# Optimization experiments

Measured on AMD Instinct MI355X. Metric: run time of the kernel, lower is better.

The kernel has to match this reference:

```python
import jax, jax.numpy as jnp
import numpy as np

B = 8192      # batch
LAT = 256     # latent_dimension
HID = 512     # hidden_size
INP = 128     # input_size (n_layer_types + 1 feature)
T = 64        # max_length
MLP = 512     # fixed MLP width in source


def _lin(key, fan_in, fan_out):
    kw, kb = jax.random.split(key)
    s = 1.0 / np.sqrt(fan_in)
    W = jax.random.uniform(kw, (fan_in, fan_out), jnp.float32, -s, s)
    b = jax.random.uniform(kb, (fan_out,), jnp.float32, -s, s)
    return W, b


def setup_inputs() -> dict:
    key = jax.random.key(0)
    ks = jax.random.split(key, 16)
    x = jax.random.normal(ks[0], (B, LAT), jnp.float32)
    W1, b1 = _lin(ks[1], LAT, MLP)
    W2, b2 = _lin(ks[2], MLP, MLP)
    W3, b3 = _lin(ks[3], MLP, MLP)
    Wh1, bh1 = _lin(ks[4], MLP, MLP)
    Wh2, bh2 = _lin(ks[5], MLP, HID)
    Wc1, bc1 = _lin(ks[6], MLP, MLP)
    Wc2, bc2 = _lin(ks[7], MLP, HID)
    Wx1, bx1 = _lin(ks[8], MLP, MLP)
    Wx2, bx2 = _lin(ks[9], MLP, INP)
    Wih, bih = _lin(ks[10], INP, 4 * HID)   # LSTM input->gates (i,f,g,o)
    Whh, bhh = _lin(ks[11], HID, 4 * HID)   # LSTM hidden->gates
    Wp, bp = _lin(ks[12], HID, INP)          # predictor head
    return dict(x=x, W1=W1, b1=b1, W2=W2, b2=b2, W3=W3, b3=b3,
                Wh1=Wh1, bh1=bh1, Wh2=Wh2, bh2=bh2,
                Wc1=Wc1, bc1=bc1, Wc2=Wc2, bc2=bc2,
                Wx1=Wx1, bx1=bx1, Wx2=Wx2, bx2=bx2,
                Wih=Wih, bih=bih, Whh=Whh, bhh=bhh, Wp=Wp, bp=bp)


def _lrelu(v):
    return jnp.where(v >= 0, v, 0.2 * v)


def _head(v):
    # split [d-1, 1]: softmax over layer types, sigmoid on feature scalar
    lt = jax.nn.softmax(v[..., :-1], axis=-1)
    ft = jax.nn.sigmoid(v[..., -1:])
    return jnp.concatenate([lt, ft], axis=-1)


def reference(x, W1, b1, W2, b2, W3, b3, Wh1, bh1, Wh2, bh2,
              Wc1, bc1, Wc2, bc2, Wx1, bx1, Wx2, bx2,
              Wih, bih, Whh, bhh, Wp, bp):
    z = _lrelu(x @ W1 + b1)
    z = _lrelu(z @ W2 + b2)
    z = _lrelu(z @ W3 + b3)
    h = _lrelu(z @ Wh1 + bh1) @ Wh2 + bh2          # [B, HID]
    c = _lrelu(z @ Wc1 + bc1) @ Wc2 + bc2          # [B, HID]
    x0 = _head(_lrelu(z @ Wx1 + bx1) @ Wx2 + bx2)  # [B, INP]

    def step(carry, _):
        xt, h, c = carry
        g = xt @ Wih + h @ Whh + (bih + bhh)        # [B, 4*HID]
        i, f, gg, o = jnp.split(g, 4, axis=-1)      # torch gate order i,f,g,o
        c2 = jax.nn.sigmoid(f) * c + jax.nn.sigmoid(i) * jnp.tanh(gg)
        h2 = jax.nn.sigmoid(o) * jnp.tanh(c2)
        nxt = _head(h2 @ Wp + bp)
        return (nxt, h2, c2), nxt

    # The torch loop reruns the LSTM over the growing prefix with the same
    # initial (h,c) and takes the last output; by LSTM causality this equals
    _, ys = jax.lax.scan(step, (x0, h, c), None, length=T)
    return jnp.transpose(ys, (1, 0, 2))  # [B, T, INP]
```

## Files before the change

kernel.cpp:

```cpp
#include <hip/hip_runtime.h>


typedef _Float16 h16;
typedef __attribute__((ext_vector_type(8))) _Float16 f16x8;
typedef __attribute__((ext_vector_type(4))) float f32x4;

#define BB 8192
#define TT 64

__device__ __forceinline__ void gload16(const void* g, void* lds) {
  __builtin_amdgcn_global_load_lds(
      (const __attribute__((address_space(1))) unsigned int*)g,
      (__attribute__((address_space(3))) unsigned int*)lds, 16, 0, 0);
}

__device__ __forceinline__ float sigm(float x) { return 1.f / (1.f + __expf(-x)); }
__device__ __forceinline__ float tanhf_(float x) { return 2.f / (1.f + __expf(-2.f * x)) - 1.f; }

#define MIDBAR_LG()                                        \
  do {                                                     \
    __builtin_amdgcn_s_barrier();                          \
    asm volatile("s_waitcnt lgkmcnt(0)" ::: "memory");     \
    __builtin_amdgcn_sched_barrier(0);                     \
  } while (0)
#define ENDBAR()                                           \
  do {                                                     \
    __builtin_amdgcn_s_barrier();                          \
    asm volatile("" ::: "memory");                         \
  } while (0)

__global__ __launch_bounds__(512, 2) void gate8(
    const h16* __restrict__ A, const h16* __restrict__ Bt,
    const float* __restrict__ bg, float* __restrict__ Cbuf,
    h16* __restrict__ Hout) {
  __shared__ __align__(16) h16 As[2][256 * 64];
  __shared__ __align__(16) h16 Bs[2][256 * 64];
  const int tid = threadIdx.x;
  const int lane = tid & 63;
  const int wid = tid >> 6;
  const int wr = wid >> 2, wc = wid & 3;
  const int m0 = blockIdx.x * 256;
  const int n0 = blockIdx.y * 256;
  const int arow = lane & 15, khi = lane >> 4;
  const int x7 = arow & 7;

  auto stage = [&](h16(*dst)[256 * 64], int slot, int h, const h16* src,
                   int base, int kt) {
#pragma unroll
    for (int li = 0; li < 2; ++li) {
      int rowbase = li * 128 + h * 64 + wid * 8;
      int row = rowbase + (lane >> 3);
      int gc = (lane & 7) ^ (lane >> 3);
      gload16(src + (size_t)(base + row) * 640 + kt * 64 + gc * 8,
              &dst[slot][rowbase * 64]);
    }
  };

  f32x4 acc[8][4];
#pragma unroll
  for (int i = 0; i < 8; ++i)
#pragma unroll
    for (int j = 0; j < 4; ++j) acc[i][j] = (f32x4)0.f;
  f16x8 af[4], bf[2][4];

  auto readA = [&](int slot, int ms, int ks) {
#pragma unroll
    for (int mr = 0; mr < 4; ++mr) {
      int r = wr * 128 + ms * 64 + mr * 16 + arow;
      af[mr] = *(const f16x8*)&As[slot][r * 64 + ((ks * 4 + khi) ^ x7) * 8];
    }
  };
  auto readB = [&](int slot, int ks) {
#pragma unroll
    for (int j = 0; j < 4; ++j) {
      int rb = wc * 64 + j * 16 + arow;
      bf[ks][j] = *(const f16x8*)&Bs[slot][rb * 64 + ((ks * 4 + khi) ^ x7) * 8];
    }
  };
  auto mfma16 = [&](int ms, int ks) {
    __builtin_amdgcn_s_setprio(1);
#pragma unroll
    for (int mr = 0; mr < 4; ++mr)
#pragma unroll
      for (int j = 0; j < 4; ++j)
        acc[ms * 4 + mr][j] = __builtin_amdgcn_mfma_f32_16x16x32_f16(
            af[mr], bf[ks][j], acc[ms * 4 + mr][j], 0, 0, 0);
    __builtin_amdgcn_s_setprio(0);
  };

  stage(Bs, 0, 0, Bt, n0, 0);
  stage(Bs, 0, 1, Bt, n0, 0);
  stage(As, 0, 0, A, m0, 0);
  stage(As, 0, 1, A, m0, 0);
  stage(Bs, 1, 0, Bt, n0, 1);
  stage(Bs, 1, 1, Bt, n0, 1);
  stage(As, 1, 0, A, m0, 1);
  asm volatile("s_waitcnt vmcnt(6)" ::: "memory");
  ENDBAR();

#pragma unroll 1
  for (int i = 0; i < 5; ++i) {
    const int t2 = 2 * i + 2, t3 = 2 * i + 3;
    readB(0, 0);
    readB(0, 1);
    readA(0, 0, 0);
    stage(As, 1, 1, A, m0, 2 * i + 1);
    MIDBAR_LG();
    mfma16(0, 0);
    ENDBAR();
    readA(0, 0, 1);
    if (t2 < 10) stage(Bs, 0, 0, Bt, n0, t2);
    MIDBAR_LG();
    mfma16(0, 1);
    ENDBAR();
    readA(0, 1, 0);
    if (t2 < 10) stage(Bs, 0, 1, Bt, n0, t2);
    MIDBAR_LG();
    mfma16(1, 0);
    ENDBAR();
    readA(0, 1, 1);
    if (t2 < 10) stage(As, 0, 0, A, m0, t2);
    if (i < 4)
      asm volatile("s_waitcnt vmcnt(6)" ::: "memory");
    else
      asm volatile("s_waitcnt vmcnt(0)" ::: "memory");
    MIDBAR_LG();
    mfma16(1, 1);
    ENDBAR();
    readB(1, 0);
    readB(1, 1);
    readA(1, 0, 0);
    if (t2 < 10) stage(As, 0, 1, A, m0, t2);
    MIDBAR_LG();
    mfma16(0, 0);
    ENDBAR();
    readA(1, 0, 1);
    if (t3 < 10) stage(Bs, 1, 0, Bt, n0, t3);
    MIDBAR_LG();
    mfma16(0, 1);
    ENDBAR();
    readA(1, 1, 0);
    if (t3 < 10) stage(Bs, 1, 1, Bt, n0, t3);
    MIDBAR_LG();
    mfma16(1, 0);
    ENDBAR();
    readA(1, 1, 1);
    if (t3 < 10) stage(As, 1, 0, A, m0, t3);
    if (i < 4)
      asm volatile("s_waitcnt vmcnt(6)" ::: "memory");
    else
      asm volatile("s_waitcnt vmcnt(0)" ::: "memory");
    MIDBAR_LG();
    mfma16(1, 1);
    ENDBAR();
  }

  const int hj = blockIdx.y * 64 + wc * 16 + arow;
  const int nb = n0 + wc * 64;
  const float bI = bg[nb + arow];
  const float bF = bg[nb + 16 + arow];
  const float bG = bg[nb + 32 + arow];
  const float bO = bg[nb + 48 + arow];
#pragma unroll
  for (int mrep = 0; mrep < 8; ++mrep) {
#pragma unroll
    for (int r = 0; r < 4; ++r) {
      int m = m0 + wr * 128 + mrep * 16 + khi * 4 + r;
      float gi = sigm(acc[mrep][0][r] + bI);
      float gf = sigm(acc[mrep][1][r] + bF);
      float gg = tanhf_(acc[mrep][2][r] + bG);
      float go = sigm(acc[mrep][3][r] + bO);
      size_t ci = (size_t)m * 512 + hj;
      float c2 = gf * Cbuf[ci] + gi * gg;
      Cbuf[ci] = c2;
      Hout[(size_t)m * 640 + 128 + hj] = (h16)(go * tanhf_(c2));
    }
  }
}

__global__ __launch_bounds__(256) void head_gemm2(
    const h16* __restrict__ A, int lda, const h16* __restrict__ Bt,
    const float* __restrict__ bias, int nkt, h16* __restrict__ Xout,
    float* __restrict__ ydst, int tstep) {
  __shared__ __align__(16) h16 As[2][64 * 64];
  __shared__ __align__(16) h16 Bs[2][128 * 64];
  const int tid = threadIdx.x;
  const int lane = tid & 63;
  const int w = tid >> 6;
  const int m0 = blockIdx.x * 64;
  const int arow = lane & 15, khi = lane >> 4;
  const int x7 = arow & 7;

  auto stageA = [&](int slot, int kt) {
#pragma unroll
    for (int li = 0; li < 2; ++li) {
      int rowbase = li * 32 + w * 8;
      int row = rowbase + (lane >> 3);
      int gc = (lane & 7) ^ (lane >> 3);
      gload16(A + (size_t)(m0 + row) * lda + kt * 64 + gc * 8,
              &As[slot][rowbase * 64]);
    }
  };
  auto stageB = [&](int slot, int kt) {
#pragma unroll
    for (int li = 0; li < 4; ++li) {
      int rowbase = li * 32 + w * 8;
      int row = rowbase + (lane >> 3);
      int gc = (lane & 7) ^ (lane >> 3);
      gload16(Bt + (size_t)row * 512 + kt * 64 + gc * 8,
              &Bs[slot][rowbase * 64]);
    }
  };

  f32x4 acc[8];
#pragma unroll
  for (int j = 0; j < 8; ++j) acc[j] = (f32x4)0.f;

  stageA(0, 0);
  stageB(0, 0);
#pragma unroll 1
  for (int kt = 0; kt < nkt; ++kt) {
    int p = kt & 1;
    if (kt + 1 < nkt) {
      stageA(p ^ 1, kt + 1);
      stageB(p ^ 1, kt + 1);
      asm volatile("s_waitcnt vmcnt(6)" ::: "memory");
    } else {
      asm volatile("s_waitcnt vmcnt(0)" ::: "memory");
    }
    ENDBAR();
#pragma unroll
    for (int kk = 0; kk < 2; ++kk) {
      int kc = kk * 4 + khi;
      int ra = w * 16 + arow;
      f16x8 afr = *(const f16x8*)&As[p][ra * 64 + (kc ^ x7) * 8];
#pragma unroll
      for (int nt = 0; nt < 8; ++nt) {
        int rb = nt * 16 + arow;
        f16x8 bfr = *(const f16x8*)&Bs[p][rb * 64 + (kc ^ x7) * 8];
        acc[nt] = __builtin_amdgcn_mfma_f32_16x16x32_f16(afr, bfr, acc[nt], 0, 0, 0);
      }
    }
    ENDBAR();
  }

#pragma unroll
  for (int r = 0; r < 4; ++r) {
    int m = m0 + w * 16 + khi * 4 + r;
    float v[8];
    float mx = -1e30f;
#pragma unroll
    for (int nt = 0; nt < 8; ++nt) {
      int col = nt * 16 + arow;
      v[nt] = acc[nt][r] + bias[col];
      if (col != 127) mx = fmaxf(mx, v[nt]);
    }
#pragma unroll
    for (int s = 1; s < 16; s <<= 1) mx = fmaxf(mx, __shfl_xor(mx, s, 16));
    float sm = 0.f;
#pragma unroll
    for (int nt = 0; nt < 8; ++nt) {
      int col = nt * 16 + arow;
      if (col != 127) sm += __expf(v[nt] - mx);
    }
#pragma unroll
    for (int s = 1; s < 16; s <<= 1) sm += __shfl_xor(sm, s, 16);
    float inv = 1.f / sm;
#pragma unroll
    for (int nt = 0; nt < 8; ++nt) {
      int col = nt * 16 + arow;
      float res = (col == 127) ? sigm(v[nt]) : __expf(v[nt] - mx) * inv;
      Xout[(size_t)m * 640 + col] = (h16)res;
      if (ydst) ydst[((size_t)m * 64 + tstep) * 128 + col] = res;
    }
  }
}

enum { EP_LRELU = 0, EP_LIN16 = 1, EP_F32 = 2 };

template <int EP>
__global__ __launch_bounds__(256) void gemm128(
    const h16* __restrict__ A, int lda, const h16* __restrict__ Bt,
    const float* __restrict__ bias, int K, h16* __restrict__ out16, int ldo,
    int ocol, float* __restrict__ outf, int ldf) {
  __shared__ __align__(16) h16 As[128 * 64];
  __shared__ __align__(16) h16 Bs[128 * 64];
  const int tid = threadIdx.x;
  const int lane = tid & 63;
  const int w = tid >> 6;
  const int m0 = blockIdx.x * 128;
  const int n0 = blockIdx.y * 128;

  f32x4 acc[4][4];
#pragma unroll
  for (int i = 0; i < 4; ++i)
#pragma unroll
    for (int j = 0; j < 4; ++j) acc[i][j] = (f32x4)0.f;

  const int rh = (w >> 1) * 64;
  const int arow = lane & 15;
  const int khi = lane >> 4;

  const int nkt = K >> 6;
  for (int kt = 0; kt < nkt; ++kt) {
#pragma unroll
    for (int li = 0; li < 4; ++li) {
      int L = w * 4 + li;
      int r = L * 8 + (lane >> 3);
      int c = lane & 7;
      int gc = c ^ (r & 7);
      gload16(A + (size_t)(m0 + r) * lda + kt * 64 + gc * 8, &As[L * 512]);
      gload16(Bt + (size_t)(n0 + r) * K + kt * 64 + gc * 8, &Bs[L * 512]);
    }
    __syncthreads();
#pragma unroll
    for (int kk = 0; kk < 2; ++kk) {
      const int kc = kk * 4 + khi;
      f16x8 af[4], bf[4];
#pragma unroll
      for (int mt = 0; mt < 4; ++mt) {
        int r = rh + mt * 16 + arow;
        af[mt] = *(const f16x8*)&As[r * 64 + (kc ^ (r & 7)) * 8];
      }
#pragma unroll
      for (int j = 0; j < 4; ++j) {
        int nt = (w & 1) * 4 + j;
        int r = nt * 16 + arow;
        bf[j] = *(const f16x8*)&Bs[r * 64 + (kc ^ (r & 7)) * 8];
      }
#pragma unroll
      for (int mt = 0; mt < 4; ++mt)
#pragma unroll
        for (int j = 0; j < 4; ++j)
          acc[mt][j] =
              __builtin_amdgcn_mfma_f32_16x16x32_f16(af[mt], bf[j], acc[mt][j], 0, 0, 0);
    }
    __syncthreads();
  }

#pragma unroll
  for (int mt = 0; mt < 4; ++mt) {
#pragma unroll
    for (int j = 0; j < 4; ++j) {
      int nt = (w & 1) * 4 + j;
      int n = n0 + nt * 16 + arow;
      float bv = bias[n];
#pragma unroll
      for (int r = 0; r < 4; ++r) {
        int m = m0 + rh + mt * 16 + khi * 4 + r;
        float v = acc[mt][j][r] + bv;
        if constexpr (EP == EP_LRELU) {
          v = v >= 0.f ? v : 0.2f * v;
          out16[(size_t)m * ldo + n] = (h16)v;
        } else if constexpr (EP == EP_LIN16) {
          out16[(size_t)m * ldo + ocol + n] = (h16)v;
        } else {
          outf[(size_t)m * ldf + n] = v;
        }
      }
    }
  }
}

__global__ void cvt16(const float* __restrict__ in, h16* __restrict__ out, int n) {
  int i = blockIdx.x * 256 + threadIdx.x;
  if (i < n) out[i] = (h16)in[i];
}

__global__ void transposeW(const float* __restrict__ W, h16* __restrict__ WT, int K,
                           int N) {
  int i = blockIdx.x * 256 + threadIdx.x;
  if (i >= K * N) return;
  int k = i / N, n = i % N;
  WT[(size_t)n * K + k] = (h16)W[i];
}

__global__ void prep_gate(const float* __restrict__ Wih, const float* __restrict__ Whh,
                          const float* __restrict__ bih, const float* __restrict__ bhh,
                          h16* __restrict__ WgT, float* __restrict__ bg) {
  int i = blockIdx.x * 256 + threadIdx.x;
  if (i >= 2048 * 640) return;
  int np = i / 640, k = i % 640;
  int by = np >> 8, wcc = (np >> 6) & 3, q = (np >> 4) & 3, jj = np & 15;
// ... 28 lines not shown
  const float* bx2 = (const float*)d_in[18];
  const float* Wih = (const float*)d_in[19];
  const float* bih = (const float*)d_in[20];
  const float* Whh = (const float*)d_in[21];
  const float* bhh = (const float*)d_in[22];
  const float* Wp = (const float*)d_in[23];
  const float* bp = (const float*)d_in[24];

  char* ws = (char*)d_ws;
  size_t off = 0;
  auto take = [&](size_t bytes) -> void* {
    void* p = ws + off;
    off += (bytes + 255) & ~(size_t)255;
    return p;
  };
  h16* X16 = (h16*)take((size_t)BB * 256 * 2);
  h16* Za = (h16*)take((size_t)BB * 512 * 2);
  h16* Zb = (h16*)take((size_t)BB * 512 * 2);
  h16* XHa = (h16*)take((size_t)BB * 640 * 2);
  h16* XHb = (h16*)take((size_t)BB * 640 * 2);
  float* C = (float*)take((size_t)BB * 512 * 4);
  h16* W1T = (h16*)take(256 * 512 * 2);
  h16* W2T = (h16*)take(512 * 512 * 2);
  h16* W3T = (h16*)take(512 * 512 * 2);
  h16* Wh1T = (h16*)take(512 * 512 * 2);
  h16* Wh2T = (h16*)take(512 * 512 * 2);
  h16* Wc1T = (h16*)take(512 * 512 * 2);
  h16* Wc2T = (h16*)take(512 * 512 * 2);
  h16* Wx1T = (h16*)take(512 * 512 * 2);
  h16* Wx2T = (h16*)take(128 * 512 * 2);
  h16* WpT = (h16*)take(128 * 512 * 2);
  h16* WgT = (h16*)take((size_t)2048 * 640 * 2);
  float* bg = (float*)take(2048 * 4);

  dim3 blk(256);
  cvt16<<<(BB * 256 + 255) / 256, blk, 0, stream>>>(x, X16, BB * 256);
  transposeW<<<(256 * 512 + 255) / 256, blk, 0, stream>>>(W1, W1T, 256, 512);
  transposeW<<<(512 * 512 + 255) / 256, blk, 0, stream>>>(W2, W2T, 512, 512);
  transposeW<<<(512 * 512 + 255) / 256, blk, 0, stream>>>(W3, W3T, 512, 512);
  transposeW<<<(512 * 512 + 255) / 256, blk, 0, stream>>>(Wh1, Wh1T, 512, 512);
  transposeW<<<(512 * 512 + 255) / 256, blk, 0, stream>>>(Wh2, Wh2T, 512, 512);
  transposeW<<<(512 * 512 + 255) / 256, blk, 0, stream>>>(Wc1, Wc1T, 512, 512);
  transposeW<<<(512 * 512 + 255) / 256, blk, 0, stream>>>(Wc2, Wc2T, 512, 512);
  transposeW<<<(512 * 512 + 255) / 256, blk, 0, stream>>>(Wx1, Wx1T, 512, 512);
  transposeW<<<(512 * 128 + 255) / 256, blk, 0, stream>>>(Wx2, Wx2T, 512, 128);
  transposeW<<<(512 * 128 + 255) / 256, blk, 0, stream>>>(Wp, WpT, 512, 128);
  prep_gate<<<(2048 * 640 + 255) / 256, blk, 0, stream>>>(Wih, Whh, bih, bhh, WgT, bg);

  gemm128<EP_LRELU><<<dim3(64, 4), blk, 0, stream>>>(X16, 256, W1T, b1, 256, Za, 512, 0, nullptr, 0);
  gemm128<EP_LRELU><<<dim3(64, 4), blk, 0, stream>>>(Za, 512, W2T, b2, 512, Zb, 512, 0, nullptr, 0);
  gemm128<EP_LRELU><<<dim3(64, 4), blk, 0, stream>>>(Zb, 512, W3T, b3, 512, Za, 512, 0, nullptr, 0);
  gemm128<EP_LRELU><<<dim3(64, 4), blk, 0, stream>>>(Za, 512, Wh1T, bh1, 512, Zb, 512, 0, nullptr, 0);
  gemm128<EP_LIN16><<<dim3(64, 4), blk, 0, stream>>>(Zb, 512, Wh2T, bh2, 512, XHa, 640, 128, nullptr, 0);
  gemm128<EP_LRELU><<<dim3(64, 4), blk, 0, stream>>>(Za, 512, Wc1T, bc1, 512, Zb, 512, 0, nullptr, 0);
  gemm128<EP_F32><<<dim3(64, 4), blk, 0, stream>>>(Zb, 512, Wc2T, bc2, 512, nullptr, 0, 0, C, 512);
  gemm128<EP_LRELU><<<dim3(64, 4), blk, 0, stream>>>(Za, 512, Wx1T, bx1, 512, Zb, 512, 0, nullptr, 0);
  head_gemm2<<<128, blk, 0, stream>>>(Zb, 512, Wx2T, bx2, 8, XHa, nullptr, 0);

  float* yout = (float*)d_out;
  for (int t = 0; t < TT; ++t) {
    h16* in_ = (t & 1) ? XHb : XHa;
    h16* out_ = (t & 1) ? XHa : XHb;
    gate8<<<dim3(32, 8), dim3(512), 0, stream>>>(in_, WgT, bg, C, out_);
    head_gemm2<<<128, blk, 0, stream>>>(out_ + 128, 640, WpT, bp, 8, out_, yout, t);
  }
}
```

Before: 2.970 ms.

## Fuse LSTM decoder time loop into persistent kernel with per-row-group barriers

Replaces the 128 per-step launches (gate GEMM plus head GEMM) with one persistent kernel of 256 blocks. The 8 blocks sharing a 256-row batch slice synchronize through atomic counters instead of kernel boundaries. Each block also runs the predictor head and softmax/sigmoid for its 32 rows in-kernel, and prefetches the next step's gate-weight tiles before waiting at the barrier. This removes launch gaps and the separate head kernel. It relies on all 256 blocks being co-resident (2 per CU), otherwise the spin barrier deadlocks.

```diff
diff --git a/kernel.cpp b/kernel.cpp
--- a/kernel.cpp
+++ b/kernel.cpp
@@ -29,23 +29,30 @@
     asm volatile("" ::: "memory");                         \
   } while (0)
 
-__global__ __launch_bounds__(512, 2) void gate8(
-    const h16* __restrict__ A, const h16* __restrict__ Bt,
-    const float* __restrict__ bg, float* __restrict__ Cbuf,
-    h16* __restrict__ Hout) {
-  __shared__ __align__(16) h16 As[2][256 * 64];
-  __shared__ __align__(16) h16 Bs[2][256 * 64];
+__global__ __launch_bounds__(512, 2) void decoder_persist(
+    h16* __restrict__ XHa, h16* __restrict__ XHb,
+    const h16* __restrict__ Bt, const float* __restrict__ bg,
+    const h16* __restrict__ WpT, const float* __restrict__ bp,
+    float* __restrict__ Cbuf, float* __restrict__ yout,
+    unsigned int* __restrict__ barcnt) {
+  __shared__ __align__(16) h16 As[2][16384];
+  __shared__ __align__(16) h16 Bs[2][16384];
   const int tid = threadIdx.x;
   const int lane = tid & 63;
   const int wid = tid >> 6;
   const int wr = wid >> 2, wc = wid & 3;
-  const int m0 = blockIdx.x * 256;
-  const int n0 = blockIdx.y * 256;
+  const int bid = blockIdx.x;
+  const int g = ((bid >> 6) << 3) | (bid & 7);
+  const int j = (bid >> 3) & 7;
+  const int m0 = g * 256;
+  const int n0 = j * 256;
   const int arow = lane & 15, khi = lane >> 4;
   const int x7 = arow & 7;
-
-  auto stage = [&](h16(*dst)[256 * 64], int slot, int h, const h16* src,
-                   int base, int kt) {
+  unsigned int* cnt = barcnt + g * 32;
+  unsigned int bargen = 0;
+
+  auto stage = [&](h16(*dst)[16384], int slot, int h, const h16* src, int base,
+                   int kt) {
 #pragma unroll
     for (int li = 0; li < 2; ++li) {
       int rowbase = li * 128 + h * 64 + wid * 8;
@@ -57,10 +64,6 @@
   };
 
   f32x4 acc[8][4];
-#pragma unroll
-  for (int i = 0; i < 8; ++i)
-#pragma unroll
-    for (int j = 0; j < 4; ++j) acc[i][j] = (f32x4)0.f;
   f16x8 af[4], bf[2][4];
 
   auto readA = [&](int slot, int ms, int ks) {
@@ -72,9 +75,9 @@
   };
   auto readB = [&](int slot, int ks) {
 #pragma unroll
-    for (int j = 0; j < 4; ++j) {
-      int rb = wc * 64 + j * 16 + arow;
-      bf[ks][j] = *(const f16x8*)&Bs[slot][rb * 64 + ((ks * 4 + khi) ^ x7) * 8];
+    for (int jj = 0; jj < 4; ++jj) {
+      int rb = wc * 64 + jj * 16 + arow;
+      bf[ks][jj] = *(const f16x8*)&Bs[slot][rb * 64 + ((ks * 4 + khi) ^ x7) * 8];
     }
   };
   auto mfma16 = [&](int ms, int ks) {
@@ -82,98 +85,208 @@
 #pragma unroll
     for (int mr = 0; mr < 4; ++mr)
 #pragma unroll
-      for (int j = 0; j < 4; ++j)
-        acc[ms * 4 + mr][j] = __builtin_amdgcn_mfma_f32_16x16x32_f16(
-            af[mr], bf[ks][j], acc[ms * 4 + mr][j], 0, 0, 0);
+      for (int jj = 0; jj < 4; ++jj)
+        acc[ms * 4 + mr][jj] = __builtin_amdgcn_mfma_f32_16x16x32_f16(
+            af[mr], bf[ks][jj], acc[ms * 4 + mr][jj], 0, 0, 0);
     __builtin_amdgcn_s_setprio(0);
   };
 
-  stage(Bs, 0, 0, Bt, n0, 0);
-  stage(Bs, 0, 1, Bt, n0, 0);
-  stage(As, 0, 0, A, m0, 0);
-  stage(As, 0, 1, A, m0, 0);
-  stage(Bs, 1, 0, Bt, n0, 1);
-  stage(Bs, 1, 1, Bt, n0, 1);
-  stage(As, 1, 0, A, m0, 1);
-  asm volatile("s_waitcnt vmcnt(6)" ::: "memory");
-  ENDBAR();
-
-#pragma unroll 1
-  for (int i = 0; i < 5; ++i) {
-    const int t2 = 2 * i + 2, t3 = 2 * i + 3;
-    readB(0, 0);
-    readB(0, 1);
-    readA(0, 0, 0);
-    stage(As, 1, 1, A, m0, 2 * i + 1);
-    MIDBAR_LG();
-    mfma16(0, 0);
-    ENDBAR();
-    readA(0, 0, 1);
-    if (t2 < 10) stage(Bs, 0, 0, Bt, n0, t2);
-    MIDBAR_LG();
-    mfma16(0, 1);
-    ENDBAR();
-    readA(0, 1, 0);
-    if (t2 < 10) stage(Bs, 0, 1, Bt, n0, t2);
-    MIDBAR_LG();
-    mfma16(1, 0);
-    ENDBAR();
-    readA(0, 1, 1);
-    if (t2 < 10) stage(As, 0, 0, A, m0, t2);
-    if (i < 4)
-      asm volatile("s_waitcnt vmcnt(6)" ::: "memory");
-    else
-      asm volatile("s_waitcnt vmcnt(0)" ::: "memory");
-    MIDBAR_LG();
-    mfma16(1, 1);
-    ENDBAR();
-    readB(1, 0);
-    readB(1, 1);
-    readA(1, 0, 0);
-    if (t2 < 10) stage(As, 0, 1, A, m0, t2);
-    MIDBAR_LG();
-    mfma16(0, 0);
-    ENDBAR();
-    readA(1, 0, 1);
-    if (t3 < 10) stage(Bs, 1, 0, Bt, n0, t3);
-    MIDBAR_LG();
-    mfma16(0, 1);
-    ENDBAR();
-    readA(1, 1, 0);
-    if (t3 < 10) stage(Bs, 1, 1, Bt, n0, t3);
-    MIDBAR_LG();
-    mfma16(1, 0);
-    ENDBAR();
-    readA(1, 1, 1);
-    if (t3 < 10) stage(As, 1, 0, A, m0, t3);
-    if (i < 4)
-      asm volatile("s_waitcnt vmcnt(6)" ::: "memory");
-    else
-      asm volatile("s_waitcnt vmcnt(0)" ::: "memory");
-    MIDBAR_LG();
-    mfma16(1, 1);
-    ENDBAR();
-  }
-
-  const int hj = blockIdx.y * 64 + wc * 16 + arow;
   const int nb = n0 + wc * 64;
   const float bI = bg[nb + arow];
   const float bF = bg[nb + 16 + arow];
   const float bG = bg[nb + 32 + arow];
   const float bO = bg[nb + 48 + arow];
-#pragma unroll
-  for (int mrep = 0; mrep < 8; ++mrep) {
-#pragma unroll
-    for (int r = 0; r < 4; ++r) {
-      int m = m0 + wr * 128 + mrep * 16 + khi * 4 + r;
-      float gi = sigm(acc[mrep][0][r] + bI);
-      float gf = sigm(acc[mrep][1][r] + bF);
-      float gg = tanhf_(acc[mrep][2][r] + bG);
-      float go = sigm(acc[mrep][3][r] + bO);
-      size_t ci = (size_t)m * 512 + hj;
-      float c2 = gf * Cbuf[ci] + gi * gg;
-      Cbuf[ci] = c2;
-      Hout[(size_t)m * 640 + 128 + hj] = (h16)(go * tanhf_(c2));
+  const int hj = j * 64 + wc * 16 + arow;
+
+#pragma unroll 1
+  for (int t = 0; t < TT; ++t) {
+    h16* Ain = (t & 1) ? XHb : XHa;
+    h16* Aout = (t & 1) ? XHa : XHb;
+
+    __syncthreads();
+    if (tid == 0)
+      __hip_atomic_fetch_add(cnt, 1u, __ATOMIC_RELEASE, __HIP_MEMORY_SCOPE_AGENT);
+    ++bargen;
+    stage(Bs, 0, 0, Bt, n0, 0);
+    stage(Bs, 0, 1, Bt, n0, 0);
+    stage(Bs, 1, 0, Bt, n0, 1);
+    stage(Bs, 1, 1, Bt, n0, 1);
+    if (tid == 0) {
+      unsigned int tgt = bargen * 8u;
+      while (__hip_atomic_load(cnt, __ATOMIC_RELAXED, __HIP_MEMORY_SCOPE_AGENT) < tgt)
+        __builtin_amdgcn_s_sleep(1);
+      __hip_atomic_fetch_add(cnt, 0u, __ATOMIC_ACQUIRE, __HIP_MEMORY_SCOPE_AGENT);
+    }
+    __syncthreads();
+
+    stage(As, 0, 0, Ain, m0, 0);
+    stage(As, 0, 1, Ain, m0, 0);
+    stage(As, 1, 0, Ain, m0, 1);
+    asm volatile("s_waitcnt vmcnt(4)" ::: "memory");
+    __builtin_amdgcn_s_barrier();
+
+#pragma unroll
+    for (int i = 0; i < 8; ++i)
+#pragma unroll
+      for (int jj = 0; jj < 4; ++jj) acc[i][jj] = (f32x4)0.f;
+
+#pragma unroll 1
+    for (int i = 0; i < 5; ++i) {
+      const int t2 = 2 * i + 2, t3 = 2 * i + 3;
+      readB(0, 0);
+      readB(0, 1);
+      readA(0, 0, 0);
+      stage(As, 1, 1, Ain, m0, 2 * i + 1);
+      MIDBAR_LG();
+      mfma16(0, 0);
+      ENDBAR();
+      readA(0, 0, 1);
+      if (t2 < 10) stage(Bs, 0, 0, Bt, n0, t2);
+      if (i == 0) asm volatile("s_waitcnt vmcnt(6)" ::: "memory");
+      MIDBAR_LG();
+      mfma16(0, 1);
+      ENDBAR();
+      readA(0, 1, 0);
+      if (t2 < 10) stage(Bs, 0, 1, Bt, n0, t2);
+      MIDBAR_LG();
+      mfma16(1, 0);
+      ENDBAR();
+      readA(0, 1, 1);
+      if (t2 < 10) stage(As, 0, 0, Ain, m0, t2);
+      if (i < 4)
+        asm volatile("s_waitcnt vmcnt(6)" ::: "memory");
+      else
+        asm volatile("s_waitcnt vmcnt(0)" ::: "memory");
+      MIDBAR_LG();
+      mfma16(1, 1);
+      ENDBAR();
+      readB(1, 0);
+      readB(1, 1);
+      readA(1, 0, 0);
+      if (t2 < 10) stage(As, 0, 1, Ain, m0, t2);
+      MIDBAR_LG();
+      mfma16(0, 0);
+      ENDBAR();
+      readA(1, 0, 1);
+      if (t3 < 10) stage(Bs, 1, 0, Bt, n0, t3);
+      MIDBAR_LG();
+      mfma16(0, 1);
+      ENDBAR();
+      readA(1, 1, 0);
+      if (t3 < 10) stage(Bs, 1, 1, Bt, n0, t3);
+      MIDBAR_LG();
+      mfma16(1, 0);
+      ENDBAR();
+      readA(1, 1, 1);
+      if (t3 < 10) stage(As, 1, 0, Ain, m0, t3);
+      if (i < 4)
+        asm volatile("s_waitcnt vmcnt(6)" ::: "memory");
+      else
+        asm volatile("s_waitcnt vmcnt(0)" ::: "memory");
+      MIDBAR_LG();
+      mfma16(1, 1);
+      ENDBAR();
+    }
+
+#pragma unroll
+    for (int mrep = 0; mrep < 8; ++mrep) {
+#pragma unroll
+      for (int r = 0; r < 4; ++r) {
+        int m = m0 + wr * 128 + mrep * 16 + khi * 4 + r;
+        float gi = sigm(acc[mrep][0][r] + bI);
+        float gf = sigm(acc[mrep][1][r] + bF);
+        float gg = tanhf_(acc[mrep][2][r] + bG);
+        float go = sigm(acc[mrep][3][r] + bO);
+        size_t ci = (size_t)m * 512 + hj;
+        float c2 = gf * Cbuf[ci] + gi * gg;
+        Cbuf[ci] = c2;
+        Aout[(size_t)m * 640 + 128 + hj] = (h16)(go * tanhf_(c2));
+      }
+    }
+
+    __syncthreads();
+    if (tid == 0)
+      __hip_atomic_fetch_add(cnt, 1u, __ATOMIC_RELEASE, __HIP_MEMORY_SCOPE_AGENT);
+    ++bargen;
+    f16x8 wfr[16];
+#pragma unroll
+    for (int kf = 0; kf < 16; ++kf)
+      wfr[kf] = *(const f16x8*)&WpT[(size_t)(wid * 16 + arow) * 512 + kf * 32 + khi * 8];
+    if (tid == 0) {
+      unsigned int tgt = bargen * 8u;
+      while (__hip_atomic_load(cnt, __ATOMIC_RELAXED, __HIP_MEMORY_SCOPE_AGENT) < tgt)
+        __builtin_amdgcn_s_sleep(1);
+      __hip_atomic_fetch_add(cnt, 0u, __ATOMIC_ACQUIRE, __HIP_MEMORY_SCOPE_AGENT);
+    }
+    __syncthreads();
+
+    {
+      h16* hst = (h16*)As;
+      float* lgs = (float*)Bs;
+      const int r0 = m0 + j * 32;
+      {
+        int row = tid >> 4;
+        int cg = tid & 15;
+        const h16* src = Aout + (size_t)(r0 + row) * 640 + 128 + cg * 32;
+#pragma unroll
+        for (int q = 0; q < 4; ++q) {
+          int c = cg * 4 + q;
+          f16x8 v = *(const f16x8*)(src + q * 8);
+          *(f16x8*)&hst[row * 512 + (c ^ (row & 7)) * 8] = v;
+        }
+      }
+      __syncthreads();
+      f32x4 hacc[2] = {(f32x4)0.f, (f32x4)0.f};
+#pragma unroll
+      for (int kf = 0; kf < 16; ++kf) {
+#pragma unroll
+        for (int mf = 0; mf < 2; ++mf) {
+          int row = mf * 16 + arow;
+          f16x8 afr = *(const f16x8*)&hst[row * 512 + ((kf * 4 + khi) ^ (row & 7)) * 8];
+          hacc[mf] = __builtin_amdgcn_mfma_f32_16x16x32_f16(afr, wfr[kf], hacc[mf], 0, 0, 0);
+        }
+      }
+#pragma unroll
+      for (int mf = 0; mf < 2; ++mf)
+#pragma unroll
+        for (int r = 0; r < 4; ++r)
+          lgs[(mf * 16 + khi * 4 + r) * 128 + wid * 16 + arow] = hacc[mf][r];
+      __syncthreads();
+      {
+        int row = tid >> 4, cg = tid & 15;
+        float v[8];
+        float mx = -1e30f;
+#pragma unroll
+        for (int q = 0; q < 8; ++q) {
+          int col = cg * 8 + q;
+          v[q] = lgs[row * 128 + col] + bp[col];
+          if (col != 127) mx = fmaxf(mx, v[q]);
+        }
+#pragma unroll
+        for (int s = 1; s < 16; s <<= 1) mx = fmaxf(mx, __shfl_xor(mx, s, 16));
+        float sm = 0.f;
+#pragma unroll
+        for (int q = 0; q < 8; ++q) {
+          int col = cg * 8 + q;
+          if (col != 127) sm += __expf(v[q] - mx);
+        }
+#pragma unroll
+        for (int s = 1; s < 16; s <<= 1) sm += __shfl_xor(sm, s, 16);
+        float inv = 1.f / sm;
+        h16 xo[8];
+        float yo[8];
+#pragma unroll
+        for (int q = 0; q < 8; ++q) {
+          int col = cg * 8 + q;
+          float res = (col == 127) ? sigm(v[q]) : __expf(v[q] - mx) * inv;
+          xo[q] = (h16)res;
+          yo[q] = res;
+        }
+        *(f16x8*)&Aout[(size_t)(r0 + row) * 640 + cg * 8] = *(f16x8*)xo;
+        float* yd = yout + (((size_t)(r0 + row)) * 64 + t) * 128 + cg * 8;
+        *(f32x4*)yd = *(f32x4*)&yo[0];
+        *(f32x4*)(yd + 4) = *(f32x4*)&yo[4];
+      }
     }
   }
 }
@@ -207,14 +320,13 @@
       int rowbase = li * 32 + w * 8;
       int row = rowbase + (lane >> 3);
       int gc = (lane & 7) ^ (lane >> 3);
-      gload16(Bt + (size_t)row * 512 + kt * 64 + gc * 8,
-              &Bs[slot][rowbase * 64]);
+      gload16(Bt + (size_t)row * 512 + kt * 64 + gc * 8, &Bs[slot][rowbase * 64]);
     }
   };
 
   f32x4 acc[8];
 #pragma unroll
-  for (int j = 0; j < 8; ++j) acc[j] = (f32x4)0.f;
+  for (int jj = 0; jj < 8; ++jj) acc[jj] = (f32x4)0.f;
 
   stageA(0, 0);
   stageB(0, 0);
@@ -295,7 +407,7 @@
 #pragma unroll
   for (int i = 0; i < 4; ++i)
 #pragma unroll
-    for (int j = 0; j < 4; ++j) acc[i][j] = (f32x4)0.f;
+    for (int jj = 0; jj < 4; ++jj) acc[i][jj] = (f32x4)0.f;
 
   const int rh = (w >> 1) * 64;
   const int arow = lane & 15;
@@ -323,17 +435,17 @@
         af[mt] = *(const f16x8*)&As[r * 64 + (kc ^ (r & 7)) * 8];
       }
 #pragma unroll
-      for (int j = 0; j < 4; ++j) {
-        int nt = (w & 1) * 4 + j;
+      for (int jj = 0; jj < 4; ++jj) {
+        int nt = (w & 1) * 4 + jj;
         int r = nt * 16 + arow;
-        bf[j] = *(const f16x8*)&Bs[r * 64 + (kc ^ (r & 7)) * 8];
+        bf[jj] = *(const f16x8*)&Bs[r * 64 + (kc ^ (r & 7)) * 8];
       }
 #pragma unroll
       for (int mt = 0; mt < 4; ++mt)
 #pragma unroll
-        for (int j = 0; j < 4; ++j)
-          acc[mt][j] =
-              __builtin_amdgcn_mfma_f32_16x16x32_f16(af[mt], bf[j], acc[mt][j], 0, 0, 0);
+        for (int jj = 0; jj < 4; ++jj)
+          acc[mt][jj] =
+              __builtin_amdgcn_mfma_f32_16x16x32_f16(af[mt], bf[jj], acc[mt][jj], 0, 0, 0);
     }
     __syncthreads();
   }
@@ -341,14 +453,14 @@
 #pragma unroll
   for (int mt = 0; mt < 4; ++mt) {
 #pragma unroll
-    for (int j = 0; j < 4; ++j) {
-      int nt = (w & 1) * 4 + j;
+    for (int jj = 0; jj < 4; ++jj) {
+      int nt = (w & 1) * 4 + jj;
       int n = n0 + nt * 16 + arow;
       float bv = bias[n];
 #pragma unroll
       for (int r = 0; r < 4; ++r) {
         int m = m0 + rh + mt * 16 + khi * 4 + r;
-        float v = acc[mt][j][r] + bv;
+        float v = acc[mt][jj][r] + bv;
         if constexpr (EP == EP_LRELU) {
           v = v >= 0.f ? v : 0.2f * v;
           out16[(size_t)m * ldo + n] = (h16)v;
@@ -443,6 +555,9 @@
   h16* WpT = (h16*)take(128 * 512 * 2);
   h16* WgT = (h16*)take((size_t)2048 * 640 * 2);
   float* bg = (float*)take(2048 * 4);
+  unsigned int* barcnt = (unsigned int*)take(32 * 32 * 4);
+
+  hipMemsetAsync(barcnt, 0, 32 * 32 * 4, stream);
 
   dim3 blk(256);
   cvt16<<<(BB * 256 + 255) / 256, blk, 0, stream>>>(x, X16, BB * 256);
@@ -468,11 +583,6 @@
   gemm128<EP_LRELU><<<dim3(64, 4), blk, 0, stream>>>(Za, 512, Wx1T, bx1, 512, Zb, 512, 0, nullptr, 0);
   head_gemm2<<<128, blk, 0, stream>>>(Zb, 512, Wx2T, bx2, 8, XHa, nullptr, 0);
 
-  float* yout = (float*)d_out;
-  for (int t = 0; t < TT; ++t) {
-    h16* in_ = (t & 1) ? XHb : XHa;
-    h16* out_ = (t & 1) ? XHa : XHb;
-    gate8<<<dim3(32, 8), dim3(512), 0, stream>>>(in_, WgT, bg, C, out_);
-    head_gemm2<<<128, blk, 0, stream>>>(out_ + 128, 640, WpT, bp, 8, out_, yout, t);
-  }
-}
+  decoder_persist<<<dim3(256), dim3(512), 0, stream>>>(
+      XHa, XHb, WgT, bg, WpT, bp, C, (float*)d_out, barcnt);
+}
```

Result: slower. 5.746 ms (+93.5%).

## Fuse predictor head GEMM into LSTM gate kernel via last-block atomic counter

Applied to the files above, without the earlier changes.

The predictor head (h @ Wp + softmax/sigmoid) is folded into the gate kernel. For each 256-row M tile, the last of the 8 N-blocks to finish, detected with a per-timestep atomic counter, computes the head for that tile. This drops one kernel launch per timestep and the re-read of h by a separate kernel. In exchange, only 32 of the 256 blocks run the head serially at the tail, which can lengthen the critical path. It also adds atomics and a memset of the counters.

```diff
diff --git a/kernel.cpp b/kernel.cpp
--- a/kernel.cpp
+++ b/kernel.cpp
@@ -32,9 +32,11 @@
 __global__ __launch_bounds__(512, 2) void gate8(
     const h16* __restrict__ A, const h16* __restrict__ Bt,
     const float* __restrict__ bg, float* __restrict__ Cbuf,
-    h16* __restrict__ Hout) {
-  __shared__ __align__(16) h16 As[2][256 * 64];
-  __shared__ __align__(16) h16 Bs[2][256 * 64];
+    h16* __restrict__ Hout, const h16* __restrict__ WpT,
+    const float* __restrict__ bp, float* __restrict__ yout, int tstep,
+    unsigned int* __restrict__ hc) {
+  __shared__ __align__(16) h16 As[2][16384];
+  __shared__ __align__(16) h16 Bs[2][16384];
   const int tid = threadIdx.x;
   const int lane = tid & 63;
   const int wid = tid >> 6;
@@ -44,8 +46,8 @@
   const int arow = lane & 15, khi = lane >> 4;
   const int x7 = arow & 7;
 
-  auto stage = [&](h16(*dst)[256 * 64], int slot, int h, const h16* src,
-                   int base, int kt) {
+  auto stage = [&](h16(*dst)[16384], int slot, int h, const h16* src, int base,
+                   int kt) {
 #pragma unroll
     for (int li = 0; li < 2; ++li) {
       int rowbase = li * 128 + h * 64 + wid * 8;
@@ -60,7 +62,7 @@
 #pragma unroll
   for (int i = 0; i < 8; ++i)
 #pragma unroll
-    for (int j = 0; j < 4; ++j) acc[i][j] = (f32x4)0.f;
+    for (int jj = 0; jj < 4; ++jj) acc[i][jj] = (f32x4)0.f;
   f16x8 af[4], bf[2][4];
 
   auto readA = [&](int slot, int ms, int ks) {
@@ -72,9 +74,9 @@
   };
   auto readB = [&](int slot, int ks) {
 #pragma unroll
-    for (int j = 0; j < 4; ++j) {
-      int rb = wc * 64 + j * 16 + arow;
-      bf[ks][j] = *(const f16x8*)&Bs[slot][rb * 64 + ((ks * 4 + khi) ^ x7) * 8];
+    for (int jj = 0; jj < 4; ++jj) {
+      int rb = wc * 64 + jj * 16 + arow;
+      bf[ks][jj] = *(const f16x8*)&Bs[slot][rb * 64 + ((ks * 4 + khi) ^ x7) * 8];
     }
   };
   auto mfma16 = [&](int ms, int ks) {
@@ -82,9 +84,9 @@
 #pragma unroll
     for (int mr = 0; mr < 4; ++mr)
 #pragma unroll
-      for (int j = 0; j < 4; ++j)
-        acc[ms * 4 + mr][j] = __builtin_amdgcn_mfma_f32_16x16x32_f16(
-            af[mr], bf[ks][j], acc[ms * 4 + mr][j], 0, 0, 0);
+      for (int jj = 0; jj < 4; ++jj)
+        acc[ms * 4 + mr][jj] = __builtin_amdgcn_mfma_f32_16x16x32_f16(
+            af[mr], bf[ks][jj], acc[ms * 4 + mr][jj], 0, 0, 0);
     __builtin_amdgcn_s_setprio(0);
   };
 
@@ -155,12 +157,12 @@
     ENDBAR();
   }
 
-  const int hj = blockIdx.y * 64 + wc * 16 + arow;
   const int nb = n0 + wc * 64;
   const float bI = bg[nb + arow];
   const float bF = bg[nb + 16 + arow];
   const float bG = bg[nb + 32 + arow];
   const float bO = bg[nb + 48 + arow];
+  const int hj = blockIdx.y * 64 + wc * 16 + arow;
 #pragma unroll
   for (int mrep = 0; mrep < 8; ++mrep) {
 #pragma unroll
@@ -174,6 +176,96 @@
       float c2 = gf * Cbuf[ci] + gi * gg;
       Cbuf[ci] = c2;
       Hout[(size_t)m * 640 + 128 + hj] = (h16)(go * tanhf_(c2));
+    }
+  }
+
+  __shared__ unsigned int lastflag;
+  __syncthreads();
+  if (tid == 0) {
+    unsigned int old = __hip_atomic_fetch_add(&hc[blockIdx.x], 1u,
+                                              __ATOMIC_ACQ_REL,
+                                              __HIP_MEMORY_SCOPE_AGENT);
+    lastflag = (old == 7u);
+  }
+  __syncthreads();
+  if (!lastflag) return;
+  __scoped_atomic_thread_fence(__ATOMIC_ACQUIRE, __MEMORY_SCOPE_DEVICE);
+
+  h16* Hlds = (h16*)As;
+  h16* Wlds = (h16*)Bs;
+  f32x4 ha[2][8];
+#pragma unroll 1
+  for (int kh = 0; kh < 2; ++kh) {
+#pragma unroll
+    for (int li = 0; li < 8; ++li) {
+      int L = wid * 8 + li;
+      int row = 2 * L + (lane >> 5);
+      int gcc = (lane & 31) ^ (row & 7);
+      gload16(WpT + (size_t)row * 512 + kh * 256 + gcc * 8, &Wlds[(2 * L) * 256]);
+    }
+#pragma unroll 1
+    for (int rh2 = 0; rh2 < 2; ++rh2) {
+#pragma unroll
+      for (int li = 0; li < 8; ++li) {
+        int L = wid * 8 + li;
+        int row = 2 * L + (lane >> 5);
+        int gcc = (lane & 31) ^ (row & 7);
+        gload16(Hout + (size_t)(m0 + rh2 * 128 + row) * 640 + 128 + kh * 256 + gcc * 8,
+                &Hlds[(2 * L) * 256]);
+      }
+      asm volatile("s_waitcnt vmcnt(0)" ::: "memory");
+      __builtin_amdgcn_s_barrier();
+      if (kh == 0) {
+#pragma unroll
+        for (int nt = 0; nt < 8; ++nt) ha[rh2][nt] = (f32x4)0.f;
+      }
+      int ra = wid * 16 + arow;
+#pragma unroll
+      for (int ks = 0; ks < 8; ++ks) {
+        f16x8 afr = *(const f16x8*)&Hlds[ra * 256 + ((ks * 4 + khi) ^ x7) * 8];
+#pragma unroll
+        for (int nt = 0; nt < 8; ++nt) {
+          int rb = nt * 16 + arow;
+          f16x8 bfr = *(const f16x8*)&Wlds[rb * 256 + ((ks * 4 + khi) ^ x7) * 8];
+          ha[rh2][nt] =
+              __builtin_amdgcn_mfma_f32_16x16x32_f16(afr, bfr, ha[rh2][nt], 0, 0, 0);
+        }
+      }
+      __builtin_amdgcn_s_barrier();
+    }
+  }
+
+#pragma unroll
+  for (int rh2 = 0; rh2 < 2; ++rh2) {
+#pragma unroll
+    for (int r = 0; r < 4; ++r) {
+      int m = m0 + rh2 * 128 + wid * 16 + khi * 4 + r;
+      float v[8];
+      float mx = -1e30f;
+#pragma unroll
+      for (int nt = 0; nt < 8; ++nt) {
+        int col = nt * 16 + arow;
+        v[nt] = ha[rh2][nt][r] + bp[col];
+        if (col != 127) mx = fmaxf(mx, v[nt]);
+      }
+#pragma unroll
+      for (int s = 1; s < 16; s <<= 1) mx = fmaxf(mx, __shfl_xor(mx, s, 16));
+      float sm = 0.f;
+#pragma unroll
+      for (int nt = 0; nt < 8; ++nt) {
+        int col = nt * 16 + arow;
+        if (col != 127) sm += __expf(v[nt] - mx);
+      }
+#pragma unroll
+      for (int s = 1; s < 16; s <<= 1) sm += __shfl_xor(sm, s, 16);
+      float inv = 1.f / sm;
+#pragma unroll
+      for (int nt = 0; nt < 8; ++nt) {
+        int col = nt * 16 + arow;
+        float res = (col == 127) ? sigm(v[nt]) : __expf(v[nt] - mx) * inv;
+        Hout[(size_t)m * 640 + col] = (h16)res;
+        yout[((size_t)m * 64 + tstep) * 128 + col] = res;
+      }
     }
   }
 }
@@ -207,14 +299,13 @@
       int rowbase = li * 32 + w * 8;
       int row = rowbase + (lane >> 3);
       int gc = (lane & 7) ^ (lane >> 3);
-      gload16(Bt + (size_t)row * 512 + kt * 64 + gc * 8,
-              &Bs[slot][rowbase * 64]);
+      gload16(Bt + (size_t)row * 512 + kt * 64 + gc * 8, &Bs[slot][rowbase * 64]);
     }
   };
 
   f32x4 acc[8];
 #pragma unroll
-  for (int j = 0; j < 8; ++j) acc[j] = (f32x4)0.f;
+  for (int jj = 0; jj < 8; ++jj) acc[jj] = (f32x4)0.f;
 
   stageA(0, 0);
   stageB(0, 0);
@@ -295,7 +386,7 @@
 #pragma unroll
   for (int i = 0; i < 4; ++i)
 #pragma unroll
-    for (int j = 0; j < 4; ++j) acc[i][j] = (f32x4)0.f;
+    for (int jj = 0; jj < 4; ++jj) acc[i][jj] = (f32x4)0.f;
 
   const int rh = (w >> 1) * 64;
   const int arow = lane & 15;
@@ -323,17 +414,17 @@
         af[mt] = *(const f16x8*)&As[r * 64 + (kc ^ (r & 7)) * 8];
       }
 #pragma unroll
-      for (int j = 0; j < 4; ++j) {
-        int nt = (w & 1) * 4 + j;
+      for (int jj = 0; jj < 4; ++jj) {
+        int nt = (w & 1) * 4 + jj;
         int r = nt * 16 + arow;
-        bf[j] = *(const f16x8*)&Bs[r * 64 + (kc ^ (r & 7)) * 8];
+        bf[jj] = *(const f16x8*)&Bs[r * 64 + (kc ^ (r & 7)) * 8];
       }
 #pragma unroll
       for (int mt = 0; mt < 4; ++mt)
 #pragma unroll
-        for (int j = 0; j < 4; ++j)
-          acc[mt][j] =
-              __builtin_amdgcn_mfma_f32_16x16x32_f16(af[mt], bf[j], acc[mt][j], 0, 0, 0);
+        for (int jj = 0; jj < 4; ++jj)
+          acc[mt][jj] =
+              __builtin_amdgcn_mfma_f32_16x16x32_f16(af[mt], bf[jj], acc[mt][jj], 0, 0, 0);
     }
     __syncthreads();
   }
@@ -341,14 +432,14 @@
 #pragma unroll
   for (int mt = 0; mt < 4; ++mt) {
 #pragma unroll
-    for (int j = 0; j < 4; ++j) {
-      int nt = (w & 1) * 4 + j;
+    for (int jj = 0; jj < 4; ++jj) {
+      int nt = (w & 1) * 4 + jj;
       int n = n0 + nt * 16 + arow;
       float bv = bias[n];
 #pragma unroll
       for (int r = 0; r < 4; ++r) {
         int m = m0 + rh + mt * 16 + khi * 4 + r;
-        float v = acc[mt][j][r] + bv;
+        float v = acc[mt][jj][r] + bv;
         if constexpr (EP == EP_LRELU) {
           v = v >= 0.f ? v : 0.2f * v;
           out16[(size_t)m * ldo + n] = (h16)v;
@@ -443,6 +534,9 @@
   h16* WpT = (h16*)take(128 * 512 * 2);
   h16* WgT = (h16*)take((size_t)2048 * 640 * 2);
   float* bg = (float*)take(2048 * 4);
+  unsigned int* hcnt = (unsigned int*)take((size_t)TT * 32 * 4);
+
+  (void)hipMemsetAsync(hcnt, 0, (size_t)TT * 32 * 4, stream);
 
   dim3 blk(256);
   cvt16<<<(BB * 256 + 255) / 256, blk, 0, stream>>>(x, X16, BB * 256);
@@ -472,7 +566,7 @@
   for (int t = 0; t < TT; ++t) {
     h16* in_ = (t & 1) ? XHb : XHa;
     h16* out_ = (t & 1) ? XHa : XHb;
-    gate8<<<dim3(32, 8), dim3(512), 0, stream>>>(in_, WgT, bg, C, out_);
-    head_gemm2<<<128, blk, 0, stream>>>(out_ + 128, 640, WpT, bp, 8, out_, yout, t);
-  }
-}
+    gate8<<<dim3(32, 8), dim3(512), 0, stream>>>(in_, WgT, bg, C, out_, WpT, bp,
+                                                 yout, t, hcnt + t * 32);
+  }
+}
```

Result: slower. 4.942 ms (+66.4%).

## Split head GEMM into 256 smaller blocks with LDS-staged vectorized softmax epilogue

Applied to the files above, without the earlier changes.

The head kernel now uses 32-row tiles, so it launches 256 blocks instead of 128, and each warp covers half the output columns. Accumulators are written to a padded LDS tile so each thread owns 16 contiguous columns of a row. This lets the softmax/sigmoid epilogue issue vectorized 16-byte stores for the fp16 next input and the fp32 output. In the time loop, block IDs are swizzled so the rows each block reads line up with the gate kernel's output tiles, aiming at better cache locality and more CU occupancy for the small per-step head. In exchange the kernel adds an extra LDS round trip and barrier, and each block loads the full weight tile twice as often.

```diff
diff --git a/kernel.cpp b/kernel.cpp
--- a/kernel.cpp
+++ b/kernel.cpp
@@ -33,8 +33,8 @@
     const h16* __restrict__ A, const h16* __restrict__ Bt,
     const float* __restrict__ bg, float* __restrict__ Cbuf,
     h16* __restrict__ Hout) {
-  __shared__ __align__(16) h16 As[2][256 * 64];
-  __shared__ __align__(16) h16 Bs[2][256 * 64];
+  __shared__ __align__(16) h16 As[2][16384];
+  __shared__ __align__(16) h16 Bs[2][16384];
   const int tid = threadIdx.x;
   const int lane = tid & 63;
   const int wid = tid >> 6;
@@ -44,8 +44,8 @@
   const int arow = lane & 15, khi = lane >> 4;
   const int x7 = arow & 7;
 
-  auto stage = [&](h16(*dst)[256 * 64], int slot, int h, const h16* src,
-                   int base, int kt) {
+  auto stage = [&](h16(*dst)[16384], int slot, int h, const h16* src, int base,
+                   int kt) {
 #pragma unroll
     for (int li = 0; li < 2; ++li) {
       int rowbase = li * 128 + h * 64 + wid * 8;
@@ -60,7 +60,7 @@
 #pragma unroll
   for (int i = 0; i < 8; ++i)
 #pragma unroll
-    for (int j = 0; j < 4; ++j) acc[i][j] = (f32x4)0.f;
+    for (int jj = 0; jj < 4; ++jj) acc[i][jj] = (f32x4)0.f;
   f16x8 af[4], bf[2][4];
 
   auto readA = [&](int slot, int ms, int ks) {
@@ -72,9 +72,9 @@
   };
   auto readB = [&](int slot, int ks) {
 #pragma unroll
-    for (int j = 0; j < 4; ++j) {
-      int rb = wc * 64 + j * 16 + arow;
-      bf[ks][j] = *(const f16x8*)&Bs[slot][rb * 64 + ((ks * 4 + khi) ^ x7) * 8];
+    for (int jj = 0; jj < 4; ++jj) {
+      int rb = wc * 64 + jj * 16 + arow;
+      bf[ks][jj] = *(const f16x8*)&Bs[slot][rb * 64 + ((ks * 4 + khi) ^ x7) * 8];
     }
   };
   auto mfma16 = [&](int ms, int ks) {
@@ -82,9 +82,9 @@
 #pragma unroll
     for (int mr = 0; mr < 4; ++mr)
 #pragma unroll
-      for (int j = 0; j < 4; ++j)
-        acc[ms * 4 + mr][j] = __builtin_amdgcn_mfma_f32_16x16x32_f16(
-            af[mr], bf[ks][j], acc[ms * 4 + mr][j], 0, 0, 0);
+      for (int jj = 0; jj < 4; ++jj)
+        acc[ms * 4 + mr][jj] = __builtin_amdgcn_mfma_f32_16x16x32_f16(
+            af[mr], bf[ks][jj], acc[ms * 4 + mr][jj], 0, 0, 0);
     __builtin_amdgcn_s_setprio(0);
   };
 
@@ -155,12 +155,12 @@
     ENDBAR();
   }
 
-  const int hj = blockIdx.y * 64 + wc * 16 + arow;
   const int nb = n0 + wc * 64;
   const float bI = bg[nb + arow];
   const float bF = bg[nb + 16 + arow];
   const float bG = bg[nb + 32 + arow];
   const float bO = bg[nb + 48 + arow];
+  const int hj = blockIdx.y * 64 + wc * 16 + arow;
 #pragma unroll
   for (int mrep = 0; mrep < 8; ++mrep) {
 #pragma unroll
@@ -178,28 +178,35 @@
   }
 }
 
-__global__ __launch_bounds__(256) void head_gemm2(
+__global__ __launch_bounds__(256) void head256(
     const h16* __restrict__ A, int lda, const h16* __restrict__ Bt,
     const float* __restrict__ bias, int nkt, h16* __restrict__ Xout,
-    float* __restrict__ ydst, int tstep) {
-  __shared__ __align__(16) h16 As[2][64 * 64];
+    float* __restrict__ ydst, int tstep, int swz) {
+  __shared__ __align__(16) h16 As[2][32 * 64];
   __shared__ __align__(16) h16 Bs[2][128 * 64];
+  __shared__ float lgs[32 * 132];
   const int tid = threadIdx.x;
   const int lane = tid & 63;
   const int w = tid >> 6;
-  const int m0 = blockIdx.x * 64;
+  const int rs = w & 1, ch = w >> 1;
   const int arow = lane & 15, khi = lane >> 4;
   const int x7 = arow & 7;
 
+  int bid = blockIdx.x;
+  int m0;
+  if (swz) {
+    int g = bid & 7, k = bid >> 3;
+    m0 = (g + 8 * (k & 3)) * 256 + (k >> 2) * 32;
+  } else {
+    m0 = bid * 32;
+  }
+
   auto stageA = [&](int slot, int kt) {
-#pragma unroll
-    for (int li = 0; li < 2; ++li) {
-      int rowbase = li * 32 + w * 8;
-      int row = rowbase + (lane >> 3);
-      int gc = (lane & 7) ^ (lane >> 3);
-      gload16(A + (size_t)(m0 + row) * lda + kt * 64 + gc * 8,
-              &As[slot][rowbase * 64]);
-    }
+    int rowbase = w * 8;
+    int gc = (lane & 7) ^ (lane >> 3);
+    int row = rowbase + (lane >> 3);
+    gload16(A + (size_t)(m0 + row) * lda + kt * 64 + gc * 8,
+            &As[slot][rowbase * 64]);
   };
   auto stageB = [&](int slot, int kt) {
 #pragma unroll
@@ -207,14 +214,13 @@
       int rowbase = li * 32 + w * 8;
       int row = rowbase + (lane >> 3);
       int gc = (lane & 7) ^ (lane >> 3);
-      gload16(Bt + (size_t)row * 512 + kt * 64 + gc * 8,
-              &Bs[slot][rowbase * 64]);
-    }
-  };
-
-  f32x4 acc[8];
-#pragma unroll
-  for (int j = 0; j < 8; ++j) acc[j] = (f32x4)0.f;
+      gload16(Bt + (size_t)row * 512 + kt * 64 + gc * 8, &Bs[slot][rowbase * 64]);
+    }
+  };
+
+  f32x4 acc[4];
+#pragma unroll
+  for (int j = 0; j < 4; ++j) acc[j] = (f32x4)0.f;
 
   stageA(0, 0);
   stageB(0, 0);
@@ -224,7 +230,7 @@
     if (kt + 1 < nkt) {
       stageA(p ^ 1, kt + 1);
       stageB(p ^ 1, kt + 1);
-      asm volatile("s_waitcnt vmcnt(6)" ::: "memory");
+      asm volatile("s_waitcnt vmcnt(5)" ::: "memory");
     } else {
       asm volatile("s_waitcnt vmcnt(0)" ::: "memory");
     }
@@ -232,46 +238,61 @@
 #pragma unroll
     for (int kk = 0; kk < 2; ++kk) {
       int kc = kk * 4 + khi;
-      int ra = w * 16 + arow;
+      int ra = rs * 16 + arow;
       f16x8 afr = *(const f16x8*)&As[p][ra * 64 + (kc ^ x7) * 8];
 #pragma unroll
-      for (int nt = 0; nt < 8; ++nt) {
-        int rb = nt * 16 + arow;
+      for (int j = 0; j < 4; ++j) {
+        int rb = (ch * 4 + j) * 16 + arow;
         f16x8 bfr = *(const f16x8*)&Bs[p][rb * 64 + (kc ^ x7) * 8];
-        acc[nt] = __builtin_amdgcn_mfma_f32_16x16x32_f16(afr, bfr, acc[nt], 0, 0, 0);
+        acc[j] = __builtin_amdgcn_mfma_f32_16x16x32_f16(afr, bfr, acc[j], 0, 0, 0);
       }
     }
     ENDBAR();
   }
 
 #pragma unroll
-  for (int r = 0; r < 4; ++r) {
-    int m = m0 + w * 16 + khi * 4 + r;
-    float v[8];
+  for (int j = 0; j < 4; ++j)
+#pragma unroll
+    for (int r = 0; r < 4; ++r)
+      lgs[(rs * 16 + khi * 4 + r) * 132 + (ch * 4 + j) * 16 + arow] = acc[j][r];
+  __syncthreads();
+  {
+    int row = tid >> 3, g8 = tid & 7;
+    float v[16];
     float mx = -1e30f;
 #pragma unroll
-    for (int nt = 0; nt < 8; ++nt) {
-      int col = nt * 16 + arow;
-      v[nt] = acc[nt][r] + bias[col];
-      if (col != 127) mx = fmaxf(mx, v[nt]);
-    }
-#pragma unroll
-    for (int s = 1; s < 16; s <<= 1) mx = fmaxf(mx, __shfl_xor(mx, s, 16));
+    for (int q = 0; q < 16; ++q) {
+      int col = g8 * 16 + q;
+      v[q] = lgs[row * 132 + col] + bias[col];
+      if (col != 127) mx = fmaxf(mx, v[q]);
+    }
+#pragma unroll
+    for (int s = 1; s < 8; s <<= 1) mx = fmaxf(mx, __shfl_xor(mx, s, 8));
     float sm = 0.f;
 #pragma unroll
-    for (int nt = 0; nt < 8; ++nt) {
-      int col = nt * 16 + arow;
-      if (col != 127) sm += __expf(v[nt] - mx);
-    }
-#pragma unroll
-    for (int s = 1; s < 16; s <<= 1) sm += __shfl_xor(sm, s, 16);
+    for (int q = 0; q < 16; ++q) {
+      int col = g8 * 16 + q;
+      if (col != 127) sm += __expf(v[q] - mx);
+    }
+#pragma unroll
+    for (int s = 1; s < 8; s <<= 1) sm += __shfl_xor(sm, s, 8);
     float inv = 1.f / sm;
-#pragma unroll
-    for (int nt = 0; nt < 8; ++nt) {
-      int col = nt * 16 + arow;
-      float res = (col == 127) ? sigm(v[nt]) : __expf(v[nt] - mx) * inv;
-      Xout[(size_t)m * 640 + col] = (h16)res;
-      if (ydst) ydst[((size_t)m * 64 + tstep) * 128 + col] = res;
+    h16 xo[16];
+    float yo[16];
+#pragma unroll
+    for (int q = 0; q < 16; ++q) {
+      int col = g8 * 16 + q;
+      float res = (col == 127) ? sigm(v[q]) : __expf(v[q] - mx) * inv;
+      xo[q] = (h16)res;
+      yo[q] = res;
+    }
+    h16* xd = Xout + (size_t)(m0 + row) * 640 + g8 * 16;
+    *(f16x8*)xd = *(f16x8*)&xo[0];
+    *(f16x8*)(xd + 8) = *(f16x8*)&xo[8];
+    if (ydst) {
+      float* yd = ydst + ((size_t)(m0 + row) * 64 + tstep) * 128 + g8 * 16;
+#pragma unroll
+      for (int q = 0; q < 4; ++q) *(f32x4*)(yd + 4 * q) = *(f32x4*)&yo[4 * q];
     }
   }
 }
@@ -295,7 +316,7 @@
 #pragma unroll
   for (int i = 0; i < 4; ++i)
 #pragma unroll
-    for (int j = 0; j < 4; ++j) acc[i][j] = (f32x4)0.f;
+    for (int jj = 0; jj < 4; ++jj) acc[i][jj] = (f32x4)0.f;
 
   const int rh = (w >> 1) * 64;
   const int arow = lane & 15;
@@ -323,17 +344,17 @@
         af[mt] = *(const f16x8*)&As[r * 64 + (kc ^ (r & 7)) * 8];
       }
 #pragma unroll
-      for (int j = 0; j < 4; ++j) {
-        int nt = (w & 1) * 4 + j;
+      for (int jj = 0; jj < 4; ++jj) {
+        int nt = (w & 1) * 4 + jj;
         int r = nt * 16 + arow;
-        bf[j] = *(const f16x8*)&Bs[r * 64 + (kc ^ (r & 7)) * 8];
+        bf[jj] = *(const f16x8*)&Bs[r * 64 + (kc ^ (r & 7)) * 8];
       }
 #pragma unroll
       for (int mt = 0; mt < 4; ++mt)
 #pragma unroll
-        for (int j = 0; j < 4; ++j)
-          acc[mt][j] =
-              __builtin_amdgcn_mfma_f32_16x16x32_f16(af[mt], bf[j], acc[mt][j], 0, 0, 0);
+        for (int jj = 0; jj < 4; ++jj)
+          acc[mt][jj] =
+              __builtin_amdgcn_mfma_f32_16x16x32_f16(af[mt], bf[jj], acc[mt][jj], 0, 0, 0);
     }
     __syncthreads();
   }
@@ -341,14 +362,14 @@
 #pragma unroll
   for (int mt = 0; mt < 4; ++mt) {
 #pragma unroll
-    for (int j = 0; j < 4; ++j) {
-      int nt = (w & 1) * 4 + j;
+    for (int jj = 0; jj < 4; ++jj) {
+      int nt = (w & 1) * 4 + jj;
       int n = n0 + nt * 16 + arow;
       float bv = bias[n];
 #pragma unroll
       for (int r = 0; r < 4; ++r) {
         int m = m0 + rh + mt * 16 + khi * 4 + r;
-        float v = acc[mt][j][r] + bv;
+        float v = acc[mt][jj][r] + bv;
         if constexpr (EP == EP_LRELU) {
           v = v >= 0.f ? v : 0.2f * v;
           out16[(size_t)m * ldo + n] = (h16)v;
@@ -466,13 +487,13 @@
   gemm128<EP_LRELU><<<dim3(64, 4), blk, 0, stream>>>(Za, 512, Wc1T, bc1, 512, Zb, 512, 0, nullptr, 0);
   gemm128<EP_F32><<<dim3(64, 4), blk, 0, stream>>>(Zb, 512, Wc2T, bc2, 512, nullptr, 0, 0, C, 512);
   gemm128<EP_LRELU><<<dim3(64, 4), blk, 0, stream>>>(Za, 512, Wx1T, bx1, 512, Zb, 512, 0, nullptr, 0);
-  head_gemm2<<<128, blk, 0, stream>>>(Zb, 512, Wx2T, bx2, 8, XHa, nullptr, 0);
+  head256<<<256, blk, 0, stream>>>(Zb, 512, Wx2T, bx2, 8, XHa, nullptr, 0, 0);
 
   float* yout = (float*)d_out;
   for (int t = 0; t < TT; ++t) {
     h16* in_ = (t & 1) ? XHb : XHa;
     h16* out_ = (t & 1) ? XHa : XHb;
     gate8<<<dim3(32, 8), dim3(512), 0, stream>>>(in_, WgT, bg, C, out_);
-    head_gemm2<<<128, blk, 0, stream>>>(out_ + 128, 640, WpT, bp, 8, out_, yout, t);
-  }
-}
+    head256<<<256, blk, 0, stream>>>(out_ + 128, 640, WpT, bp, 8, out_, yout, t, 1);
+  }
+}
```

Result: faster. 2.839 ms (-4.4%).
